# Kernel optimization log

Hardware: AMD Instinct MI355X
Metric: run time of the kernel (lower is better)

## Reference

```python
import jax, jax.numpy as jnp
import numpy as np

HEADS = 8
UNITS = 1024
D_ATT = UNITS // HEADS  # 128
NEG_INF = -1e9  # matches Keras Attention additive causal mask


def setup_inputs() -> dict:
    key = jax.random.key(0)
    kx, kq, kk, kv, ko = jax.random.split(key, 5)
    B, T = 4, 2048
    scale = 0.02
    x = jax.random.normal(kx, (B, T, UNITS), dtype=jnp.float32)
    Wq = jax.random.normal(kq, (UNITS, HEADS * D_ATT), dtype=jnp.float32) * scale
    Wk = jax.random.normal(kk, (UNITS, HEADS * D_ATT), dtype=jnp.float32) * scale
    Wv = jax.random.normal(kv, (UNITS, D_ATT), dtype=jnp.float32) * scale
    Wo = jax.random.normal(ko, (D_ATT, UNITS), dtype=jnp.float32) * scale
    return {"x": x, "Wq": Wq, "Wk": Wk, "Wv": Wv, "Wo": Wo}


def reference(x, Wq, Wk, Wv, Wo):
    # TFT interpretable multi-head self-attention (inference; dropout inactive).
    B, T, U = x.shape
    H, d = HEADS, D_ATT
    scale = 1.0 / jnp.sqrt(jnp.asarray(d, x.dtype))  # query / sqrt(shape(key)[-1])
    q = (x @ Wq).reshape(B, T, H, d) * scale          # [B,T,H,d]
    k = (x @ Wk).reshape(B, T, H, d)                  # [B,T,H,d]
    v = x @ Wv                                        # [B,T,d], shared across heads
    scores = jnp.einsum("bthd,bshd->bhts", q, k)      # [B,H,T,T]
    causal = jnp.tril(jnp.ones((T, T), dtype=bool))   # [T,T]
    scores = jnp.where(causal, scores, jnp.asarray(NEG_INF, scores.dtype))
    w = jax.nn.softmax(scores, axis=-1)               # [B,H,T,T]
    out = jnp.einsum("bhts,bsd->bthd", w, v)          # [B,T,H,d]
    out = out.mean(axis=2) @ Wo                       # mean over heads -> Dense(units)
    attn = w.mean(axis=1)                             # mean attention over heads [B,T,T]
    return out, attn
```

## Files before the change

### kernel.cpp

```cpp
#include <hip/hip_runtime.h>

#define BATCH 4
#define TSEQ  2048
#define UNITS 1024
#define HEADS 8
#define DH    128
#define MROWS (BATCH*TSEQ)
#define NCAT  (2*UNITS + DH)

typedef short bf16x8 __attribute__((ext_vector_type(8)));
typedef short short4v __attribute__((ext_vector_type(4)));
typedef float f32x4  __attribute__((ext_vector_type(4)));

__device__ __forceinline__ short f2bf(float f){
    union { float f; unsigned u; } v; v.f = f;
    unsigned r = v.u + 0x7fff + ((v.u >> 16) & 1);
    return (short)(r >> 16);
}
__device__ __forceinline__ float redsum16(float v){
    #pragma unroll
    for (int m = 1; m < 16; m <<= 1) v += __shfl_xor(v, m);
    return v;
}
__device__ __forceinline__ void gload_lds16(const void* g, void* l){
    __builtin_amdgcn_global_load_lds(
        (const __attribute__((address_space(1))) void*)g,
        (__attribute__((address_space(3))) void*)l, 16, 0, 0);
}

#define QSCALE (0.08838834764831845f * 1.4426950408889634f)

__global__ __launch_bounds__(256) void xcast_kernel(const float* __restrict__ x,
                                                    short* __restrict__ Xbf)
{
    const int N = MROWS*UNITS/8;
    for (int i = blockIdx.x*256 + threadIdx.x; i < N; i += gridDim.x*256){
        f32x4 a = *(const f32x4*)(x + (size_t)i*8);
        f32x4 b = *(const f32x4*)(x + (size_t)i*8 + 4);
        bf16x8 o;
        o[0]=f2bf(a[0]); o[1]=f2bf(a[1]); o[2]=f2bf(a[2]); o[3]=f2bf(a[3]);
        o[4]=f2bf(b[0]); o[5]=f2bf(b[1]); o[6]=f2bf(b[2]); o[7]=f2bf(b[3]);
        *(bf16x8*)(Xbf + (size_t)i*8) = o;
    }
}

__global__ __launch_bounds__(256) void wtrans_kernel(
    const float* __restrict__ Wq, const float* __restrict__ Wk,
    const float* __restrict__ Wv, const float* __restrict__ Wo,
    short* __restrict__ WT, short* __restrict__ WoT)
{
    __shared__ float T_lds[64][65];
    const int tid = threadIdx.x;
    const int bid = blockIdx.x;
    if (bid < 544){
        const int nt = bid >> 4, kt = bid & 15;
        const int n0 = nt*64, k0 = kt*64;
        const float* src; int scol; float sc = 1.0f; int sstride = UNITS;
        if (n0 < UNITS){ src = Wq; scol = n0; sc = QSCALE; }
        else if (n0 < 2*UNITS){ src = Wk; scol = n0 - UNITS; }
        else { src = Wv; scol = n0 - 2*UNITS; sstride = DH; }
        const int ln = tid & 63, lk0 = tid >> 6;
        for (int kk = lk0; kk < 64; kk += 4)
            T_lds[kk][ln] = src[(size_t)(k0+kk)*sstride + scol + ln] * sc;
        __syncthreads();
        const int lk = tid & 63, ln0 = tid >> 6;
        for (int nn = ln0; nn < 64; nn += 4)
            WT[(size_t)(n0+nn)*UNITS + k0 + lk] = f2bf(T_lds[lk][nn]);
    } else {
        const int t = bid - 544;
        const int nt = t >> 1, dt = t & 1;
        const int n0 = nt*64, d0 = dt*64;
        const int ln = tid & 63, lk0 = tid >> 6;
        for (int dd = lk0; dd < 64; dd += 4)
            T_lds[dd][ln] = Wo[(size_t)(d0+dd)*UNITS + n0 + ln];
        __syncthreads();
        const int ld = tid & 63, ln0 = tid >> 6;
        for (int nn = ln0; nn < 64; nn += 4)
            WoT[(size_t)(n0+nn)*DH + d0 + ld] = f2bf(T_lds[ld][nn]);
    }
}

__global__ __launch_bounds__(256) void gemm_qkv_kernel(
    const short* __restrict__ X, const short* __restrict__ WT,
    short* __restrict__ Qbf, short* __restrict__ Kbf, short* __restrict__ Vt)
{
    __shared__ short A_lds[128][32];
    __shared__ short B_lds[128][32];
    const int tid = threadIdx.x;
    const int w = tid >> 6, l = tid & 63, lg = l >> 4, lr = l & 15;
    const int wm = w >> 1, wn = w & 1;
    const int n0 = blockIdx.x * 128;
    const int m0 = blockIdx.y * 128;
    const f32x4 fzero = {0.f, 0.f, 0.f, 0.f};
    f32x4 acc[4][4];
    #pragma unroll
    for (int i = 0; i < 4; i++)
        #pragma unroll
        for (int j = 0; j < 4; j++) acc[i][j] = fzero;

    const int srow = (l >> 2);
    const int scol = (l & 3) * 8;

    for (int k0 = 0; k0 < UNITS; k0 += 32){
        #pragma unroll
        for (int i = 0; i < 2; i++){
            int row = w*32 + i*16 + srow;
            gload_lds16(X  + (size_t)(m0+row)*UNITS + k0 + scol,
                        (char*)A_lds + ((w*2 + i) << 10));
            gload_lds16(WT + (size_t)(n0+row)*UNITS + k0 + scol,
                        (char*)B_lds + ((w*2 + i) << 10));
        }
        __syncthreads();
        bf16x8 af[4], bfr[4];
        #pragma unroll
        for (int mf = 0; mf < 4; mf++)
            af[mf] = *(const bf16x8*)(&A_lds[wm*64 + mf*16 + lr][lg*8]);
        #pragma unroll
        for (int nf = 0; nf < 4; nf++)
            bfr[nf] = *(const bf16x8*)(&B_lds[wn*64 + nf*16 + lr][lg*8]);
        #pragma unroll
        for (int mf = 0; mf < 4; mf++)
            #pragma unroll
            for (int nf = 0; nf < 4; nf++)
                acc[mf][nf] = __builtin_amdgcn_mfma_f32_16x16x32_bf16(
                    af[mf], bfr[nf], acc[mf][nf], 0, 0, 0);
        __syncthreads();
    }

    #pragma unroll
    for (int mf = 0; mf < 4; mf++){
        #pragma unroll
        for (int nf = 0; nf < 4; nf++){
            #pragma unroll
            for (int r = 0; r < 4; r++){
                int gr = m0 + wm*64 + mf*16 + lg*4 + r;
                int gc = n0 + wn*64 + nf*16 + lr;
                int b = gr >> 11, t = gr & 2047;
                short v = f2bf(acc[mf][nf][r]);
                if (gc < UNITS){
                    int h = gc >> 7, dd = gc & 127;
                    Qbf[(((size_t)(b*HEADS + h))*TSEQ + t)*DH + dd] = v;
                } else if (gc < 2*UNITS){
                    int h = (gc - UNITS) >> 7, dd = gc & 127;
                    Kbf[(((size_t)(b*HEADS + h))*TSEQ + t)*DH + dd] = v;
                } else {
                    int dd = gc - 2*UNITS;
                    Vt[((size_t)b*DH + dd)*TSEQ + t] = v;
                }
            }
        }
    }
}

__global__ __launch_bounds__(256) void stats_kernel(
    const short* __restrict__ Qbf, const short* __restrict__ Kbf,
    float* __restrict__ Lb)
{
    __shared__ short K_lds[64][136];
    const int tid = threadIdx.x;
    const int w = tid >> 6, l = tid & 63, lg = l >> 4, lr = l & 15;
    const int bh = blockIdx.y;
    const int qt = 31 - blockIdx.x;
    const int q0 = qt * 64;
    const short* Qh = Qbf + (size_t)bh*TSEQ*DH;
    const short* Kh = Kbf + (size_t)bh*TSEQ*DH;
    const f32x4 fzero = {0.f, 0.f, 0.f, 0.f};

    const int qrow = q0 + w*16 + lr;
    bf16x8 aq[4];
    #pragma unroll
    for (int ks = 0; ks < 4; ks++)
        aq[ks] = *(const bf16x8*)(Qh + (size_t)qrow*DH + ks*32 + lg*8);

    float lrow[4] = {0.f, 0.f, 0.f, 0.f};

    for (int kv0 = 0; kv0 <= q0; kv0 += 64){
        #pragma unroll
        for (int i = 0; i < 4; i++){
            int c = tid + i*256;
            int row = c >> 4, c8 = c & 15;
            *(bf16x8*)(&K_lds[row][c8*8]) =
                *(const bf16x8*)(Kh + (size_t)(kv0+row)*DH + c8*8);
        }
        __syncthreads();
        f32x4 sacc[4];
        #pragma unroll
        for (int nf = 0; nf < 4; nf++) sacc[nf] = fzero;
        __builtin_amdgcn_s_setprio(1);
        #pragma unroll
        for (int ks = 0; ks < 4; ks++){
            #pragma unroll
            for (int nf = 0; nf < 4; nf++){
                bf16x8 kb = *(const bf16x8*)(&K_lds[nf*16 + lr][ks*32 + lg*8]);
                sacc[nf] = __builtin_amdgcn_mfma_f32_16x16x32_bf16(aq[ks], kb, sacc[nf], 0,0,0);
            }
        }
        __builtin_amdgcn_s_setprio(0);
        if (kv0 == q0){
            #pragma unroll
            for (int nf = 0; nf < 4; nf++)
                #pragma unroll
                for (int r = 0; r < 4; r++)
                    if (nf*16 + lr > w*16 + lg*4 + r) sacc[nf][r] = -1e30f;
        }
        #pragma unroll
        for (int r = 0; r < 4; r++)
            lrow[r] += (exp2f(sacc[0][r]) + exp2f(sacc[1][r]))
                     + (exp2f(sacc[2][r]) + exp2f(sacc[3][r]));
        __syncthreads();
    }
    #pragma unroll
    for (int r = 0; r < 4; r++) lrow[r] = redsum16(lrow[r]);
    if (lr == 0){
        #pragma unroll
        for (int r = 0; r < 4; r++){
            int t = q0 + w*16 + lg*4 + r;
            Lb[(size_t)bh*TSEQ + t] = 1.0f / lrow[r];
        }
    }
}

__global__ __launch_bounds__(256) void attn_kernel(
    const short* __restrict__ Qbf, const short* __restrict__ Kbf,
    const float* __restrict__ Lb, float* __restrict__ attn)
{
    const int tid = threadIdx.x;
    const int b = blockIdx.y;
    const int qt = blockIdx.x >> 5, kt = blockIdx.x & 31;
    const int q0 = qt*64, k0 = kt*64;
    float* At = attn + (size_t)b*TSEQ*TSEQ;

    if (kt > qt){
        const f32x4 fz = {0.f, 0.f, 0.f, 0.f};
        #pragma unroll
        for (int i = 0; i < 4; i++){
            int c = tid + i*256;
            int row = c >> 4, c4 = c & 15;
            *(f32x4*)(At + (size_t)(q0+row)*TSEQ + k0 + c4*4) = fz;
        }
        return;
    }

    __shared__ short Q_lds[64][136];
    __shared__ short K_lds2[64][136];
    const int w = tid >> 6, l = tid & 63, lg = l >> 4, lr = l & 15;
    const f32x4 fzero = {0.f, 0.f, 0.f, 0.f};

    float wacc[4][4] = {};
    for (int h = 0; h < HEADS; h++){
        const short* Qh = Qbf + ((size_t)(b*HEADS + h))*TSEQ*DH;
        const short* Kh = Kbf + ((size_t)(b*HEADS + h))*TSEQ*DH;
        #pragma unroll
        for (int i = 0; i < 4; i++){
            int c = tid + i*256;
            int row = c >> 4, c8 = c & 15;
            *(bf16x8*)(&Q_lds[row][c8*8]) =
                *(const bf16x8*)(Qh + (size_t)(q0+row)*DH + c8*8);
            *(bf16x8*)(&K_lds2[row][c8*8]) =
                *(const bf16x8*)(Kh + (size_t)(k0+row)*DH + c8*8);
        }
        __syncthreads();
        float rlh[4];
        #pragma unroll
        for (int r = 0; r < 4; r++){
            int t = q0 + w*16 + lg*4 + r;
            rlh[r] = Lb[((size_t)(b*HEADS + h))*TSEQ + t];
        }
        f32x4 sacc[4];
        #pragma unroll
        for (int nf = 0; nf < 4; nf++) sacc[nf] = fzero;
        __builtin_amdgcn_s_setprio(1);
        #pragma unroll
        for (int ks = 0; ks < 4; ks++){
            bf16x8 a = *(const bf16x8*)(&Q_lds[w*16 + lr][ks*32 + lg*8]);
            #pragma unroll
            for (int nf = 0; nf < 4; nf++){
                bf16x8 bb = *(const bf16x8*)(&K_lds2[nf*16 + lr][ks*32 + lg*8]);
                sacc[nf] = __builtin_amdgcn_mfma_f32_16x16x32_bf16(a, bb, sacc[nf], 0,0,0);
            }
        }
        __builtin_amdgcn_s_setprio(0);
        #pragma unroll
        for (int nf = 0; nf < 4; nf++)
            #pragma unroll
            for (int r = 0; r < 4; r++){
                int qg = q0 + w*16 + lg*4 + r;
                int sg = k0 + nf*16 + lr;
                float v = (sg <= qg) ? exp2f(sacc[nf][r]) * rlh[r] : 0.f;
                wacc[nf][r] += v;
            }
        __syncthreads();
    }
    #pragma unroll
    for (int nf = 0; nf < 4; nf++)
        #pragma unroll
        for (int r = 0; r < 4; r++){
            int qg = q0 + w*16 + lg*4 + r;
            int sg = k0 + nf*16 + lr;
            At[(size_t)qg*TSEQ + sg] = wacc[nf][r] * 0.125f;
        }
}

__global__ __launch_bounds__(256) void pv_kernel(
    const float* __restrict__ attn, const short* __restrict__ Vt,
    float* __restrict__ Obuf)
{
    __shared__ short A_lds[64][72];
    __shared__ short V_lds[128][72];
    const int tid = threadIdx.x;
    const int w = tid >> 6, l = tid & 63, lg = l >> 4, lr = l & 15;
    const int mt = blockIdx.x;
    const int ks0 = blockIdx.y;
    const int b = blockIdx.z;
    const int m0 = mt*64;
    const int kmax = m0 + 64;
    const int kbeg = ks0*512;
    if (kbeg >= kmax) return;
    const int kend = min(kbeg + 512, kmax);
    const int nact = (kmax + 511) >> 9;
    const float* Ab = attn + (size_t)b*TSEQ*TSEQ;
    const short* Vb = Vt + (size_t)b*DH*TSEQ;
    const f32x4 fzero = {0.f, 0.f, 0.f, 0.f};
    f32x4 acc[8];
    #pragma unroll
    for (int i = 0; i < 8; i++) acc[i] = fzero;

    for (int k0 = kbeg; k0 < kend; k0 += 64){
        #pragma unroll
        for (int i = 0; i < 4; i++){
            int c = tid + i*256;
            int row = c >> 4, c4 = c & 15;
            f32x4 av = *(const f32x4*)(Ab + (size_t)(m0+row)*TSEQ + k0 + c4*4);
            short4v o;
            o[0]=f2bf(av[0]); o[1]=f2bf(av[1]); o[2]=f2bf(av[2]); o[3]=f2bf(av[3]);
            *(short4v*)(&A_lds[row][c4*4]) = o;
        }
        #pragma unroll
        for (int i = 0; i < 4; i++){
            int c = tid + i*256;
            int row = c >> 3, c8 = c & 7;
            *(bf16x8*)(&V_lds[row][c8*8]) =
                *(const bf16x8*)(Vb + (size_t)row*TSEQ + k0 + c8*8);
        }
        __syncthreads();
        __builtin_amdgcn_s_setprio(1);
        #pragma unroll
        for (int ks = 0; ks < 2; ks++){
            bf16x8 a = *(const bf16x8*)(&A_lds[w*16 + lr][ks*32 + lg*8]);
            #pragma unroll
            for (int cg = 0; cg < 8; cg++){
                bf16x8 vb = *(const bf16x8*)(&V_lds[cg*16 + lr][ks*32 + lg*8]);
                acc[cg] = __builtin_amdgcn_mfma_f32_16x16x32_bf16(a, vb, acc[cg], 0,0,0);
            }
        }
        __builtin_amdgcn_s_setprio(0);
        __syncthreads();
    }
    #pragma unroll
    for (int cg = 0; cg < 8; cg++)
        #pragma unroll
        for (int r = 0; r < 4; r++){
            int row = m0 + w*16 + lg*4 + r, col = cg*16 + lr;
            float* p = &Obuf[((size_t)b*TSEQ + row)*DH + col];
            if (nact == 1) *p = acc[cg][r];
            else atomicAdd(p, acc[cg][r]);
        }
}

__global__ __launch_bounds__(256) void gemm_out_kernel(
    const float* __restrict__ Ob, const short* __restrict__ WoT,
    float* __restrict__ out)
{
    __shared__ short A_lds[128][40];
    __shared__ short B_lds[128][40];
    const int tid = threadIdx.x;
    const int w = tid >> 6, l = tid & 63, lg = l >> 4, lr = l & 15;
    const int wm = w >> 1, wn = w & 1;
    const int n0 = blockIdx.x * 128;
    const int m0 = blockIdx.y * 128;
    const f32x4 fzero = {0.f, 0.f, 0.f, 0.f};
    f32x4 acc[4][4];
    #pragma unroll
    for (int i = 0; i < 4; i++)
        #pragma unroll
        for (int j = 0; j < 4; j++) acc[i][j] = fzero;

    for (int k0 = 0; k0 < DH; k0 += 32){
        #pragma unroll
        for (int i = 0; i < 2; i++){
            int c = tid + i*256;
            int row = c >> 2, c8 = c & 3;
            f32x4 a0 = *(const f32x4*)(Ob + (size_t)(m0+row)*DH + k0 + c8*8);
            f32x4 a1 = *(const f32x4*)(Ob + (size_t)(m0+row)*DH + k0 + c8*8 + 4);
            bf16x8 o;
            o[0]=f2bf(a0[0]); o[1]=f2bf(a0[1]); o[2]=f2bf(a0[2]); o[3]=f2bf(a0[3]);
            o[4]=f2bf(a1[0]); o[5]=f2bf(a1[1]); o[6]=f2bf(a1[2]); o[7]=f2bf(a1[3]);
            *(bf16x8*)(&A_lds[row][c8*8]) = o;
            *(bf16x8*)(&B_lds[row][c8*8]) =
                *(const bf16x8*)(WoT + (size_t)(n0+row)*DH + k0 + c8*8);
        }
        __syncthreads();
        bf16x8 af[4], bfr[4];
        #pragma unroll
        for (int mf = 0; mf < 4; mf++)
            af[mf] = *(const bf16x8*)(&A_lds[wm*64 + mf*16 + lr][lg*8]);
        #pragma unroll
        for (int nf = 0; nf < 4; nf++)
            bfr[nf] = *(const bf16x8*)(&B_lds[wn*64 + nf*16 + lr][lg*8]);
        #pragma unroll
        for (int mf = 0; mf < 4; mf++)
            #pragma unroll
            for (int nf = 0; nf < 4; nf++)
                acc[mf][nf] = __builtin_amdgcn_mfma_f32_16x16x32_bf16(
                    af[mf], bfr[nf], acc[mf][nf], 0, 0, 0);
        __syncthreads();
    }
    #pragma unroll
    for (int mf = 0; mf < 4; mf++)
        #pragma unroll
        for (int nf = 0; nf < 4; nf++)
            #pragma unroll
            for (int r = 0; r < 4; r++){
                int gr = m0 + wm*64 + mf*16 + lg*4 + r;
                int gc = n0 + wn*64 + nf*16 + lr;
                out[(size_t)gr*UNITS + gc] = acc[mf][nf][r];
            }
}

extern "C" void kernel_launch(void* const* d_in, const int* in_sizes, int n_in,
                              void* d_out, int out_size, void* d_ws, size_t ws_size,
                              hipStream_t stream)
{
    const float* x  = (const float*)d_in[0];
    const float* Wq = (const float*)d_in[1];
    const float* Wk = (const float*)d_in[2];
    const float* Wv = (const float*)d_in[3];
    const float* Wo = (const float*)d_in[4];
    float* out  = (float*)d_out;
    float* attn = out + (size_t)MROWS*UNITS;

    char* ws = (char*)d_ws;
    short* Xbf = (short*)(ws);
    short* WT  = (short*)(ws + 16777216);
    short* Qbf = (short*)(ws + 21233664);
    short* Kbf = (short*)(ws + 38010880);
    short* Vt  = (short*)(ws + 54788096);
    float* Lb  = (float*)(ws + 57147392);
    short* WoT = (short*)(ws + 57409536);
    float* Obuf = (float*)ws;

    xcast_kernel<<<2048, 256, 0, stream>>>(x, Xbf);
    wtrans_kernel<<<576, 256, 0, stream>>>(Wq, Wk, Wv, Wo, WT, WoT);
    gemm_qkv_kernel<<<dim3(NCAT/128, MROWS/128), 256, 0, stream>>>(Xbf, WT, Qbf, Kbf, Vt);
    hipMemsetAsync(Obuf, 0, (size_t)MROWS*DH*sizeof(float), stream);
    stats_kernel<<<dim3(TSEQ/64, BATCH*HEADS), 256, 0, stream>>>(Qbf, Kbf, Lb);
    attn_kernel<<<dim3(32*32, BATCH), 256, 0, stream>>>(Qbf, Kbf, Lb, attn);
    pv_kernel<<<dim3(TSEQ/64, 4, BATCH), 256, 0, stream>>>(attn, Vt, Obuf);
    gemm_out_kernel<<<dim3(UNITS/128, MROWS/128), 256, 0, stream>>>(Obuf, WoT, out);
}
```

Baseline: 379.0 us.

## Double-buffer K tiles and enlarge attention-weight tiles to 128 query rows

The stats kernel now prefetches the next K tile into registers while computing on the current one, using a double-buffered LDS tile, so each iteration needs one barrier instead of two. The attention-weights kernel is retiled to 128 query rows per block. Q is loaded straight into registers and K is double-buffered across heads. Output tiles are staged through LDS so the global stores are coalesced as float4 rows. The goal is to hide global load latency and to reuse each K tile across more query rows, at the cost of more registers and possibly lower occupancy.

```diff
diff --git a/kernel.cpp b/kernel.cpp
--- a/kernel.cpp
+++ b/kernel.cpp
@@ -156,7 +156,7 @@
     const short* __restrict__ Qbf, const short* __restrict__ Kbf,
     float* __restrict__ Lb)
 {
-    __shared__ short K_lds[64][136];
+    __shared__ short K_lds[2][64][136];
     const int tid = threadIdx.x;
     const int w = tid >> 6, l = tid & 63, lg = l >> 4, lr = l & 15;
     const int bh = blockIdx.y;
@@ -166,23 +166,34 @@
     const short* Kh = Kbf + (size_t)bh*TSEQ*DH;
     const f32x4 fzero = {0.f, 0.f, 0.f, 0.f};
 
+    const int srow = tid >> 4;
+    const int sc8  = tid & 15;
+
     const int qrow = q0 + w*16 + lr;
     bf16x8 aq[4];
     #pragma unroll
     for (int ks = 0; ks < 4; ks++)
         aq[ks] = *(const bf16x8*)(Qh + (size_t)qrow*DH + ks*32 + lg*8);
 
+    bf16x8 kreg[4];
+    #pragma unroll
+    for (int i = 0; i < 4; i++)
+        kreg[i] = *(const bf16x8*)(Kh + (size_t)(srow + i*16)*DH + sc8*8);
+    #pragma unroll
+    for (int i = 0; i < 4; i++)
+        *(bf16x8*)(&K_lds[0][srow + i*16][sc8*8]) = kreg[i];
+    __syncthreads();
+
     float lrow[4] = {0.f, 0.f, 0.f, 0.f};
-
-    for (int kv0 = 0; kv0 <= q0; kv0 += 64){
-        #pragma unroll
-        for (int i = 0; i < 4; i++){
-            int c = tid + i*256;
-            int row = c >> 4, c8 = c & 15;
-            *(bf16x8*)(&K_lds[row][c8*8]) =
-                *(const bf16x8*)(Kh + (size_t)(kv0+row)*DH + c8*8);
-        }
-        __syncthreads();
+    const int ntile = qt + 1;
+    for (int t = 0; t < ntile; t++){
+        const int cur = t & 1;
+        if (t + 1 < ntile){
+            const size_t base = (size_t)((t+1)*64 + srow)*DH + sc8*8;
+            #pragma unroll
+            for (int i = 0; i < 4; i++)
+                kreg[i] = *(const bf16x8*)(Kh + base + (size_t)i*16*DH);
+        }
         f32x4 sacc[4];
         #pragma unroll
         for (int nf = 0; nf < 4; nf++) sacc[nf] = fzero;
@@ -191,12 +202,12 @@
         for (int ks = 0; ks < 4; ks++){
             #pragma unroll
             for (int nf = 0; nf < 4; nf++){
-                bf16x8 kb = *(const bf16x8*)(&K_lds[nf*16 + lr][ks*32 + lg*8]);
+                bf16x8 kb = *(const bf16x8*)(&K_lds[cur][nf*16 + lr][ks*32 + lg*8]);
                 sacc[nf] = __builtin_amdgcn_mfma_f32_16x16x32_bf16(aq[ks], kb, sacc[nf], 0,0,0);
             }
         }
         __builtin_amdgcn_s_setprio(0);
-        if (kv0 == q0){
+        if (t == qt){
             #pragma unroll
             for (int nf = 0; nf < 4; nf++)
                 #pragma unroll
@@ -207,6 +218,11 @@
         for (int r = 0; r < 4; r++)
             lrow[r] += (exp2f(sacc[0][r]) + exp2f(sacc[1][r]))
                      + (exp2f(sacc[2][r]) + exp2f(sacc[3][r]));
+        if (t + 1 < ntile){
+            #pragma unroll
+            for (int i = 0; i < 4; i++)
+                *(bf16x8*)(&K_lds[cur ^ 1][srow + i*16][sc8*8]) = kreg[i];
+        }
         __syncthreads();
     }
     #pragma unroll
@@ -226,14 +242,14 @@
 {
     const int tid = threadIdx.x;
     const int b = blockIdx.y;
-    const int qt = blockIdx.x >> 5, kt = blockIdx.x & 31;
-    const int q0 = qt*64, k0 = kt*64;
+    const int qt = blockIdx.x >> 5, kvt = blockIdx.x & 31;
+    const int q0 = qt*128, k0 = kvt*64;
     float* At = attn + (size_t)b*TSEQ*TSEQ;
 
-    if (kt > qt){
+    if (k0 > q0 + 127){
         const f32x4 fz = {0.f, 0.f, 0.f, 0.f};
         #pragma unroll
-        for (int i = 0; i < 4; i++){
+        for (int i = 0; i < 8; i++){
             int c = tid + i*256;
             int row = c >> 4, c4 = c & 15;
             *(f32x4*)(At + (size_t)(q0+row)*TSEQ + k0 + c4*4) = fz;
@@ -241,64 +257,102 @@
         return;
     }
 
-    __shared__ short Q_lds[64][136];
-    __shared__ short K_lds2[64][136];
+    __shared__ short K_lds[2][64][136];
     const int w = tid >> 6, l = tid & 63, lg = l >> 4, lr = l & 15;
+    const int srow = tid >> 4, sc8 = tid & 15;
     const f32x4 fzero = {0.f, 0.f, 0.f, 0.f};
-
-    float wacc[4][4] = {};
+    const size_t bh0 = (size_t)(b*HEADS)*TSEQ*DH;
+
+    bf16x8 kreg[4];
+    {
+        const short* Kh = Kbf + bh0;
+        #pragma unroll
+        for (int i = 0; i < 4; i++)
+            kreg[i] = *(const bf16x8*)(Kh + (size_t)(k0 + srow + i*16)*DH + sc8*8);
+        #pragma unroll
+        for (int i = 0; i < 4; i++)
+            *(bf16x8*)(&K_lds[0][srow + i*16][sc8*8]) = kreg[i];
+    }
+    __syncthreads();
+
+    f32x4 wacc[2][4];
+    #pragma unroll
+    for (int qf = 0; qf < 2; qf++)
+        #pragma unroll
+        for (int nf = 0; nf < 4; nf++) wacc[qf][nf] = fzero;
+
     for (int h = 0; h < HEADS; h++){
-        const short* Qh = Qbf + ((size_t)(b*HEADS + h))*TSEQ*DH;
-        const short* Kh = Kbf + ((size_t)(b*HEADS + h))*TSEQ*DH;
-        #pragma unroll
-        for (int i = 0; i < 4; i++){
-            int c = tid + i*256;
-            int row = c >> 4, c8 = c & 15;
-            *(bf16x8*)(&Q_lds[row][c8*8]) =
-                *(const bf16x8*)(Qh + (size_t)(q0+row)*DH + c8*8);
-            *(bf16x8*)(&K_lds2[row][c8*8]) =
-                *(const bf16x8*)(Kh + (size_t)(k0+row)*DH + c8*8);
-        }
-        __syncthreads();
-        float rlh[4];
-        #pragma unroll
-        for (int r = 0; r < 4; r++){
-            int t = q0 + w*16 + lg*4 + r;
-            rlh[r] = Lb[((size_t)(b*HEADS + h))*TSEQ + t];
-        }
-        f32x4 sacc[4];
-        #pragma unroll
-        for (int nf = 0; nf < 4; nf++) sacc[nf] = fzero;
+        const int cur = h & 1;
+        if (h + 1 < HEADS){
+            const short* Kn = Kbf + bh0 + (size_t)(h+1)*TSEQ*DH;
+            #pragma unroll
+            for (int i = 0; i < 4; i++)
+                kreg[i] = *(const bf16x8*)(Kn + (size_t)(k0 + srow + i*16)*DH + sc8*8);
+        }
+        const short* Qh = Qbf + bh0 + (size_t)h*TSEQ*DH;
+        bf16x8 aq[2][4];
+        #pragma unroll
+        for (int qf = 0; qf < 2; qf++)
+            #pragma unroll
+            for (int ks = 0; ks < 4; ks++)
+                aq[qf][ks] = *(const bf16x8*)(Qh + (size_t)(q0 + w*32 + qf*16 + lr)*DH + ks*32 + lg*8);
+
+        f32x4 sacc[2][4];
+        #pragma unroll
+        for (int qf = 0; qf < 2; qf++)
+            #pragma unroll
+            for (int nf = 0; nf < 4; nf++) sacc[qf][nf] = fzero;
         __builtin_amdgcn_s_setprio(1);
         #pragma unroll
         for (int ks = 0; ks < 4; ks++){
-            bf16x8 a = *(const bf16x8*)(&Q_lds[w*16 + lr][ks*32 + lg*8]);
             #pragma unroll
             for (int nf = 0; nf < 4; nf++){
-                bf16x8 bb = *(const bf16x8*)(&K_lds2[nf*16 + lr][ks*32 + lg*8]);
-                sacc[nf] = __builtin_amdgcn_mfma_f32_16x16x32_bf16(a, bb, sacc[nf], 0,0,0);
+                bf16x8 kb = *(const bf16x8*)(&K_lds[cur][nf*16 + lr][ks*32 + lg*8]);
+                sacc[0][nf] = __builtin_amdgcn_mfma_f32_16x16x32_bf16(aq[0][ks], kb, sacc[0][nf], 0,0,0);
+                sacc[1][nf] = __builtin_amdgcn_mfma_f32_16x16x32_bf16(aq[1][ks], kb, sacc[1][nf], 0,0,0);
             }
         }
         __builtin_amdgcn_s_setprio(0);
+
+        const float* Lh = Lb + ((size_t)(b*HEADS + h))*TSEQ;
+        #pragma unroll
+        for (int qf = 0; qf < 2; qf++){
+            f32x4 rlh = *(const f32x4*)(Lh + q0 + w*32 + qf*16 + lg*4);
+            #pragma unroll
+            for (int nf = 0; nf < 4; nf++){
+                #pragma unroll
+                for (int r = 0; r < 4; r++){
+                    int row = q0 + w*32 + qf*16 + lg*4 + r;
+                    int col = k0 + nf*16 + lr;
+                    float v = (col <= row) ? exp2f(sacc[qf][nf][r]) * rlh[r] : 0.f;
+                    wacc[qf][nf][r] += v;
+                }
+            }
+        }
+        if (h + 1 < HEADS){
+            #pragma unroll
+            for (int i = 0; i < 4; i++)
+                *(bf16x8*)(&K_lds[cur ^ 1][srow + i*16][sc8*8]) = kreg[i];
+        }
+        __syncthreads();
+    }
+
+    float* ob = (float*)&K_lds[0][0][0];
+    #pragma unroll
+    for (int qf = 0; qf < 2; qf++)
         #pragma unroll
         for (int nf = 0; nf < 4; nf++)
             #pragma unroll
-            for (int r = 0; r < 4; r++){
-                int qg = q0 + w*16 + lg*4 + r;
-                int sg = k0 + nf*16 + lr;
-                float v = (sg <= qg) ? exp2f(sacc[nf][r]) * rlh[r] : 0.f;
-                wacc[nf][r] += v;
-            }
-        __syncthreads();
-    }
-    #pragma unroll
-    for (int nf = 0; nf < 4; nf++)
-        #pragma unroll
-        for (int r = 0; r < 4; r++){
-            int qg = q0 + w*16 + lg*4 + r;
-            int sg = k0 + nf*16 + lr;
-            At[(size_t)qg*TSEQ + sg] = wacc[nf][r] * 0.125f;
-        }
+            for (int r = 0; r < 4; r++)
+                ob[(w*32 + qf*16 + lg*4 + r)*68 + nf*16 + lr] = wacc[qf][nf][r] * 0.125f;
+    __syncthreads();
+    #pragma unroll
+    for (int i = 0; i < 8; i++){
+        int c = tid + i*256;
+        int row = c >> 4, c4 = c & 15;
+        *(f32x4*)(At + (size_t)(q0+row)*TSEQ + k0 + c4*4) =
+            *(const f32x4*)(ob + row*68 + c4*4);
+    }
 }
 
 __global__ __launch_bounds__(256) void pv_kernel(
@@ -454,7 +508,7 @@
     gemm_qkv_kernel<<<dim3(NCAT/128, MROWS/128), 256, 0, stream>>>(Xbf, WT, Qbf, Kbf, Vt);
     hipMemsetAsync(Obuf, 0, (size_t)MROWS*DH*sizeof(float), stream);
     stats_kernel<<<dim3(TSEQ/64, BATCH*HEADS), 256, 0, stream>>>(Qbf, Kbf, Lb);
-    attn_kernel<<<dim3(32*32, BATCH), 256, 0, stream>>>(Qbf, Kbf, Lb, attn);
+    attn_kernel<<<dim3(16*32, BATCH), 256, 0, stream>>>(Qbf, Kbf, Lb, attn);
     pv_kernel<<<dim3(TSEQ/64, 4, BATCH), 256, 0, stream>>>(attn, Vt, Obuf);
     gemm_out_kernel<<<dim3(UNITS/128, MROWS/128), 256, 0, stream>>>(Obuf, WoT, out);
 }
```

Result: slower. 388.7 us (+2.6%).
